# Kernel optimization log

Measured on AMD Instinct MI355X. Metric: run time of the kernel, lower is better.

## Reference

```python
import jax, jax.numpy as jnp
import numpy as np

B, H, W = 2, 256, 256


def _fwd_diff(x, ax):
    # forward difference with Neumann boundary (last entry = 0)
    pad = [(0, 0)] * x.ndim
    pad[ax] = (0, 1)
    return jnp.pad(jnp.diff(x, axis=ax), pad)


def _bwd_div(x, ax):
    # exact adjoint: <_fwd_diff(u), x> = -<u, _bwd_div(x)>
    sl = [slice(None)] * x.ndim
    sl[ax] = slice(0, -1)
    pad_end = [(0, 0)] * x.ndim
    pad_end[ax] = (0, 1)
    x0 = jnp.pad(x[tuple(sl)], pad_end)  # zero out last entry along ax
    pad_front = [(0, 0)] * x.ndim
    pad_front[ax] = (1, 0)
    shifted = jnp.pad(x0[tuple(sl)], pad_front)
    return x0 - shifted


def _grad(u):  # (B,H,W) -> (B,H,W,2)
    return jnp.stack([_fwd_diff(u, 1), _fwd_diff(u, 2)], axis=-1)


def _div(p):  # (B,H,W,2) -> (B,H,W)
    return _bwd_div(p[..., 0], 1) + _bwd_div(p[..., 1], 2)


def _sym_grad(v):  # (B,H,W,2) -> (B,H,W,3): (e11, e22, e12)
    v1, v2 = v[..., 0], v[..., 1]
    e11 = _fwd_diff(v1, 1)
    e22 = _fwd_diff(v2, 2)
    e12 = 0.5 * (_fwd_diff(v1, 2) + _fwd_diff(v2, 1))
    return jnp.stack([e11, e22, e12], axis=-1)


def _sym_div(q):  # adjoint of _sym_grad (with e12 counted twice)
    c1 = _bwd_div(q[..., 0], 1) + _bwd_div(q[..., 2], 2)
    c2 = _bwd_div(q[..., 2], 1) + _bwd_div(q[..., 1], 2)
    return jnp.stack([c1, c2], axis=-1)


def _proj_ball(p, alpha, weights):
    # pointwise projection onto {||p|| <= alpha} with weighted euclidean norm
    n = jnp.sqrt(jnp.sum(weights * p * p, axis=-1, keepdims=True))
    return p / jnp.maximum(1.0, n / alpha)


def _tgv_pdhg(u0, alpha0, alpha1, num_iters):
    # Chambolle-Pock PDHG for second-order TGV-regularized L2 denoising:
    #   min_u 0.5*||u - f||^2 + TGV_{alpha0,alpha1}(u)
    f = u0
    L = jnp.sqrt(12.0).astype(u0.dtype)  # ||K||^2 <= 12 for the TGV operator
    tau = 1.0 / L
    sigma = 1.0 / L
    v0 = jnp.zeros((*u0.shape, 2), u0.dtype)
    p0 = jnp.zeros((*u0.shape, 2), u0.dtype)  # matches p=zeros((*u.shape,2)) in the net
    q0 = jnp.zeros((*u0.shape, 3), u0.dtype)
    w1 = jnp.asarray([1.0, 1.0], u0.dtype)
    w2 = jnp.asarray([1.0, 1.0, 2.0], u0.dtype)  # off-diagonal counted twice

    @jax.checkpoint
    def step(carry, _):
        u, u_bar, v, v_bar, p, q = carry
        # dual ascent + projections
        p = _proj_ball(p + sigma * (_grad(u_bar) - v_bar), alpha1, w1)
        q = _proj_ball(q + sigma * _sym_grad(v_bar), alpha0, w2)
        # primal descent; prox of 0.5||u-f||^2
        u_new = (u + tau * _div(p) + tau * f) / (1.0 + tau)
        v_new = v + tau * (p + _sym_div(q))
        # over-relaxation (theta = 1)
        return (u_new, 2.0 * u_new - u, v_new, 2.0 * v_new - v, p, q), None

    carry0 = (u0, u0, v0, v0, p0, q0)
    (u_T, _, _, _, _, _), _ = jax.lax.scan(step, carry0, None, length=num_iters)
    return u_T


def setup_inputs() -> dict:
    key = jax.random.key(0)
    u = jax.random.normal(key, (B, H, W), dtype=jnp.float32)
    # the module hard-codes [0.1, 0.1] as the two regularisation parameters
    regularisation_params = jnp.array([0.1, 0.1], dtype=jnp.float32)
    return {"u": u, "regularisation_params": regularisation_params, "T": 128}


def reference(u, regularisation_params, T):
    alpha0 = regularisation_params[0]
    alpha1 = regularisation_params[1]
    return _tgv_pdhg(u, alpha0, alpha1, T)
```

## Files before the change

kernel.cpp:

```cpp
#include <hip/hip_runtime.h>
#include <math.h>


namespace {

typedef float v2f __attribute__((ext_vector_type(2)));

constexpr int kN = 2 * 256 * 256;
constexpr float kTau = 0.28867513459481287f;
constexpr float kSigma = kTau;
constexpr float kInv1pTau = 1.0f / (1.0f + kTau);

constexpr int RR = 32;
constexpr int RC = 48;
constexpr int A = RR * RC;
constexpr int PAD = 64;
constexpr int TILE_R = 16;
constexpr int TILE_C = 32;
constexpr int HALO = 8;
constexpr int NLAUNCH = 128 / HALO;
constexpr int NTHREADS = RR * (RC / 2);

__device__ __forceinline__ float4 ld4(const float* p) {
  return *reinterpret_cast<const float4*>(p);
}

template <bool M>
__device__ __forceinline__ void run8(
    float* ubS, float* vbS, float* p1S, float* p2S, float* q11S, float* q22S,
    float* q12S, const int rc, const int r, const float alpha0,
    const float alpha1, const float mD, const float mU, const v2f mR,
    const v2f mL, const v2f fI, v2f& u_, v2f& ub_, v2f& v1_, v2f& v2_,
    v2f& vb1_, v2f& vb2_, v2f& p1_, v2f& p2_, v2f& q11_, v2f& q22_,
    v2f& q12_) {
  for (int t = 0; t < HALO; ++t) {
    const bool pubD = (r >= t) && (r <= 31 - t);
    const bool actD = (r >= t) && (r <= 30 - t);
    const bool actP = (r >= t + 1) && (r <= 30 - t);

    if (pubD) {
      *reinterpret_cast<v2f*>(ubS + rc) = ub_;
      float4 vp;
      vp.x = vb1_.x; vp.y = vb2_.x; vp.z = vb1_.y; vp.w = vb2_.y;
      *reinterpret_cast<float4*>(vbS + 2 * rc) = vp;
    }
    __syncthreads();

    if (actD) {
      const float ubX = ubS[rc + 2];
      const v2f vbX = *reinterpret_cast<const v2f*>(vbS + 2 * (rc + 2));
      const v2f ubD = *reinterpret_cast<const v2f*>(ubS + rc + RC);
      const float4 vd = ld4(vbS + 2 * (rc + RC));
      v2f vb1D, vb2D;
      vb1D.x = vd.x; vb1D.y = vd.z;
      vb2D.x = vd.y; vb2D.y = vd.w;

      v2f ubr, vb1r, vb2r;
      ubr.x = ub_.y;   ubr.y = ubX;
      vb1r.x = vb1_.y; vb1r.y = vbX.x;
      vb2r.x = vb2_.y; vb2r.y = vbX.y;

      const v2f du1 = M ? mD * (ubD - ub_) : (ubD - ub_);
      const v2f du2 = M ? mR * (ubr - ub_) : (ubr - ub_);
      const v2f pn1 = p1_ + kSigma * (du1 - vb1_);
      const v2f pn2 = p2_ + kSigma * (du2 - vb2_);
      const v2f n2p = pn1 * pn1 + pn2 * pn2;
      v2f sp;
      sp.x = fminf(1.f, alpha1 * __builtin_amdgcn_rsqf(n2p.x));
      sp.y = fminf(1.f, alpha1 * __builtin_amdgcn_rsqf(n2p.y));
      p1_ = pn1 * sp;
      p2_ = pn2 * sp;

      const v2f e11 = M ? mD * (vb1D - vb1_) : (vb1D - vb1_);
      const v2f e22 = M ? mR * (vb2r - vb2_) : (vb2r - vb2_);
      const v2f e12 = M ? 0.5f * (mR * (vb1r - vb1_) + mD * (vb2D - vb2_))
                        : 0.5f * ((vb1r - vb1_) + (vb2D - vb2_));
      const v2f qn1 = q11_ + kSigma * e11;
      const v2f qn2 = q22_ + kSigma * e22;
      const v2f qn3 = q12_ + kSigma * e12;
      const v2f n2q = qn1 * qn1 + qn2 * qn2 + 2.f * (qn3 * qn3);
      v2f sq;
      sq.x = fminf(1.f, alpha0 * __builtin_amdgcn_rsqf(n2q.x));
      sq.y = fminf(1.f, alpha0 * __builtin_amdgcn_rsqf(n2q.y));
      q11_ = qn1 * sq;
      q22_ = qn2 * sq;
      q12_ = qn3 * sq;

      *reinterpret_cast<v2f*>(p1S + rc) = p1_;
      *reinterpret_cast<v2f*>(p2S + rc) = p2_;
      *reinterpret_cast<v2f*>(q11S + rc) = q11_;
      *reinterpret_cast<v2f*>(q22S + rc) = q22_;
      *reinterpret_cast<v2f*>(q12S + rc) = q12_;
    }
    __syncthreads();

    if (actP) {
      const v2f p1U = *reinterpret_cast<const v2f*>(p1S + rc - RC);
      const v2f q11U = *reinterpret_cast<const v2f*>(q11S + rc - RC);
      const v2f q12U = *reinterpret_cast<const v2f*>(q12S + rc - RC);
      const float p2Ls = p2S[rc - 1];
      const float q22Ls = q22S[rc - 1];
      const float q12Ls = q12S[rc - 1];

      v2f p2l, q22l, q12l;
      p2l.x = p2Ls;   p2l.y = p2_.x;
      q22l.x = q22Ls; q22l.y = q22_.x;
      q12l.x = q12Ls; q12l.y = q12_.x;

      const v2f divp = M ? (mD * p1_ + mR * p2_ - (mU * p1U + mL * p2l))
                         : (p1_ + p2_ - (p1U + p2l));
      const v2f un = (u_ + kTau * divp + fI) * kInv1pTau;
      ub_ = 2.f * un - u_;
      u_ = un;

      const v2f c1 = M ? (mD * q11_ + mR * q12_ - (mU * q11U + mL * q12l))
                       : (q11_ + q12_ - (q11U + q12l));
      const v2f c2 = M ? (mD * q12_ + mR * q22_ - (mU * q12U + mL * q22l))
                       : (q12_ + q22_ - (q12U + q22l));
      const v2f v1n = v1_ + kTau * (p1_ + c1);
      const v2f v2n = v2_ + kTau * (p2_ + c2);
      vb1_ = 2.f * v1n - v1_;
      v1_ = v1n;
      vb2_ = 2.f * v2n - v2_;
      v2_ = v2n;
    }
  }
}

__global__ __launch_bounds__(NTHREADS, 3) void tgv8_kernel(
    const float* __restrict__ f, const float* __restrict__ rp,
    float* __restrict__ ug, float* __restrict__ ws, int t0) {
  float* pr0 = ws + 0 * 2 * kN;
  float* pr1 = ws + 1 * 2 * kN;
  float* pr2 = ws + 2 * 2 * kN;
  float* pr3 = ws + 3 * 2 * kN;
  float* pr4 = ws + 4 * 2 * kN;

  __shared__ __align__(16) float smem[PAD + 8 * A + PAD];
  float* ubS = smem + PAD;
  float* vbS = ubS + A;
  float* p1S = vbS + 2 * A;
  float* p2S = p1S + A;
  float* q11S = p2S + A;
  float* q22S = q11S + A;
  float* q12S = q22S + A;

  const int lin = blockIdx.x + 8 * (blockIdx.y + 16 * blockIdx.z);
  const int j = ((lin & 7) << 5) | (lin >> 3);
  const int bz = j >> 7;
  const int by = (j >> 3) & 15;
  const int bx = j & 7;

  const int tid = threadIdx.x;
  const int r = tid / 24;
  const int c = (tid % 24) * 2;
  const int rc = r * RC + c;

  const int gi = by * TILE_R + r - HALO;
  const int gj = bx * TILE_C + c - HALO;
  const bool inImg = ((unsigned)gi < 256u) && ((unsigned)gj < 256u);
  const int base = bz * 65536 + gi * 256 + gj;

  const bool interior = (bx >= 1) && (bx <= 6) && (by >= 1) && (by <= 14);

  const float alpha0 = rp[0];
  const float alpha1 = rp[1];

  const float mD = (gi != 255) ? 1.f : 0.f;
  const float mU = (gi != 0) ? 1.f : 0.f;
  v2f mR, mL;
  mR.x = (gj + 0 != 255) ? 1.f : 0.f;
  mR.y = (gj + 1 != 255) ? 1.f : 0.f;
  mL.x = (gj != 0) ? 1.f : 0.f;
  mL.y = 1.f;

  v2f u_, ub_, v1_, v2_, vb1_, vb2_, p1_, p2_, q11_, q22_, q12_, f_;

#define LOADP(va, vb, src)                    \
  {                                           \
    const float4 t4 = ld4((src) + 2 * base);  \
    va.x = t4.x; vb.x = t4.y;                 \
    va.y = t4.z; vb.y = t4.w;                 \
  }
  if (inImg) {
    f_ = *reinterpret_cast<const v2f*>(f + base);
    if (t0 == 0) {
      u_ = f_; ub_ = f_;
      v1_ = 0.f; v2_ = 0.f; vb1_ = 0.f; vb2_ = 0.f;
      p1_ = 0.f; p2_ = 0.f; q11_ = 0.f; q22_ = 0.f; q12_ = 0.f;
    } else {
      LOADP(ub_, q12_, pr3)
      LOADP(vb1_, vb2_, pr0)
      LOADP(p1_, p2_, pr1)
      LOADP(q11_, q22_, pr2)
      u_ = *reinterpret_cast<const v2f*>(ug + base);
      LOADP(v1_, v2_, pr4)
    }
  } else {
    f_ = 0.f; u_ = 0.f; ub_ = 0.f;
    v1_ = 0.f; v2_ = 0.f; vb1_ = 0.f; vb2_ = 0.f;
    p1_ = 0.f; p2_ = 0.f; q11_ = 0.f; q22_ = 0.f; q12_ = 0.f;
  }
#undef LOADP

  const v2f fI = kTau * f_;

  if (interior) {
    run8<false>(ubS, vbS, p1S, p2S, q11S, q22S, q12S, rc, r, alpha0, alpha1,
                mD, mU, mR, mL, fI, u_, ub_, v1_, v2_, vb1_, vb2_, p1_, p2_,
                q11_, q22_, q12_);
  } else {
    run8<true>(ubS, vbS, p1S, p2S, q11S, q22S, q12S, rc, r, alpha0, alpha1,
               mD, mU, mR, mL, fI, u_, ub_, v1_, v2_, vb1_, vb2_, p1_, p2_,
               q11_, q22_, q12_);
  }

  if (r >= HALO && r < HALO + TILE_R && c >= HALO && c < HALO + TILE_C) {
#define STOREP(va, vb, dst)                              \
  {                                                      \
    float4 t4;                                           \
    t4.x = va.x; t4.y = vb.x; t4.z = va.y; t4.w = vb.y;  \
    *reinterpret_cast<float4*>((dst) + 2 * base) = t4;   \
  }
    *reinterpret_cast<v2f*>(ug + base) = u_;
    if (t0 != NLAUNCH - 1) {
      STOREP(vb1_, vb2_, pr0)
      STOREP(p1_, p2_, pr1)
      STOREP(q11_, q22_, pr2)
      STOREP(ub_, q12_, pr3)
      STOREP(v1_, v2_, pr4)
    }
#undef STOREP
  }
}

}

extern "C" void kernel_launch(void* const* d_in, const int* in_sizes, int n_in,
                              void* d_out, int out_size, void* d_ws,
                              size_t ws_size, hipStream_t stream) {
  const float* f = (const float*)d_in[0];
  const float* rp = (const float*)d_in[1];

  float* u = (float*)d_out;
  float* ws = (float*)d_ws;

  dim3 grid(256 / TILE_C, 256 / TILE_R, 2);
  for (int t = 0; t < NLAUNCH; ++t) {
    hipLaunchKernelGGL(tgv8_kernel, grid, dim3(NTHREADS), 0, stream, f, rp, u,
                       ws, t);
  }
}
```

Measured before the change: 199.3 us.

## Replace block barriers with neighbor-wave shared-memory flag synchronization

Replaces the two __syncthreads per time step with point-to-point flags in LDS: each wavefront publishes its step counter and spins only on the adjacent wavefront whose rows it reads. To map one row pair per wave, the block is widened to 32x32 threads with 8 idle lanes per row and launch bounds lowered to 1 block per CU. This removes full-block barrier stalls but wastes a quarter of the lanes, lowers occupancy, and relies on volatile spin-waits and waitcnt ordering being correct.

```diff
diff --git a/kernel.cpp b/kernel.cpp
--- a/kernel.cpp
+++ b/kernel.cpp
@@ -19,7 +19,7 @@
 constexpr int TILE_C = 32;
 constexpr int HALO = 8;
 constexpr int NLAUNCH = 128 / HALO;
-constexpr int NTHREADS = RR * (RC / 2);
+constexpr int NTHREADS = 32 * 32;
 
 __device__ __forceinline__ float4 ld4(const float* p) {
   return *reinterpret_cast<const float4*>(p);
@@ -28,15 +28,16 @@
 template <bool M>
 __device__ __forceinline__ void run8(
     float* ubS, float* vbS, float* p1S, float* p2S, float* q11S, float* q22S,
-    float* q12S, const int rc, const int r, const float alpha0,
-    const float alpha1, const float mD, const float mU, const v2f mR,
-    const v2f mL, const v2f fI, v2f& u_, v2f& ub_, v2f& v1_, v2f& v2_,
-    v2f& vb1_, v2f& vb2_, v2f& p1_, v2f& p2_, v2f& q11_, v2f& q22_,
+    float* q12S, volatile int* vA, volatile int* vB, const int w,
+    const int lane, const bool active, const int rc, const int r,
+    const float alpha0, const float alpha1, const float mD, const float mU,
+    const v2f mR, const v2f mL, const v2f fI, v2f& u_, v2f& ub_, v2f& v1_,
+    v2f& v2_, v2f& vb1_, v2f& vb2_, v2f& p1_, v2f& p2_, v2f& q11_, v2f& q22_,
     v2f& q12_) {
   for (int t = 0; t < HALO; ++t) {
-    const bool pubD = (r >= t) && (r <= 31 - t);
-    const bool actD = (r >= t) && (r <= 30 - t);
-    const bool actP = (r >= t + 1) && (r <= 30 - t);
+    const bool pubD = active && (r >= t) && (r <= 31 - t);
+    const bool actD = active && (r >= t) && (r <= 30 - t);
+    const bool actP = active && (r >= t + 1) && (r <= 30 - t);
 
     if (pubD) {
       *reinterpret_cast<v2f*>(ubS + rc) = ub_;
@@ -44,7 +45,13 @@
       vp.x = vb1_.x; vp.y = vb2_.x; vp.z = vb1_.y; vp.w = vb2_.y;
       *reinterpret_cast<float4*>(vbS + 2 * rc) = vp;
     }
-    __syncthreads();
+    asm volatile("s_waitcnt lgkmcnt(0)" ::: "memory");
+    if (lane == 0) vA[w] = t;
+    if (w < 15) {
+      while (vA[w + 1] < t) {
+      }
+    }
+    __builtin_amdgcn_sched_barrier(0);
 
     if (actD) {
       const float ubX = ubS[rc + 2];
@@ -92,7 +99,13 @@
       *reinterpret_cast<v2f*>(q22S + rc) = q22_;
       *reinterpret_cast<v2f*>(q12S + rc) = q12_;
     }
-    __syncthreads();
+    asm volatile("s_waitcnt lgkmcnt(0)" ::: "memory");
+    if (lane == 0) vB[w] = t;
+    if (w > 0) {
+      while (vB[w - 1] < t) {
+      }
+    }
+    __builtin_amdgcn_sched_barrier(0);
 
     if (actP) {
       const v2f p1U = *reinterpret_cast<const v2f*>(p1S + rc - RC);
@@ -127,7 +140,7 @@
   }
 }
 
-__global__ __launch_bounds__(NTHREADS, 3) void tgv8_kernel(
+__global__ __launch_bounds__(NTHREADS, 1) void tgv8_kernel(
     const float* __restrict__ f, const float* __restrict__ rp,
     float* __restrict__ ug, float* __restrict__ ws, int t0) {
   float* pr0 = ws + 0 * 2 * kN;
@@ -137,6 +150,8 @@
   float* pr4 = ws + 4 * 2 * kN;
 
   __shared__ __align__(16) float smem[PAD + 8 * A + PAD];
+  __shared__ int flagA[16];
+  __shared__ int flagB[16];
   float* ubS = smem + PAD;
   float* vbS = ubS + A;
   float* p1S = vbS + 2 * A;
@@ -152,13 +167,23 @@
   const int bx = j & 7;
 
   const int tid = threadIdx.x;
-  const int r = tid / 24;
-  const int c = (tid % 24) * 2;
+  const int r = tid >> 5;
+  const int s = tid & 31;
+  const bool active = (s < 24);
+  const int c = s * 2;
   const int rc = r * RC + c;
+  const int w = tid >> 6;
+  const int lane = tid & 63;
+
+  if (tid < 16) {
+    flagA[tid] = -1;
+    flagB[tid] = -1;
+  }
+  __syncthreads();
 
   const int gi = by * TILE_R + r - HALO;
   const int gj = bx * TILE_C + c - HALO;
-  const bool inImg = ((unsigned)gi < 256u) && ((unsigned)gj < 256u);
+  const bool inImg = active && ((unsigned)gi < 256u) && ((unsigned)gj < 256u);
   const int base = bz * 65536 + gi * 256 + gj;
 
   const bool interior = (bx >= 1) && (bx <= 6) && (by >= 1) && (by <= 14);
@@ -206,13 +231,13 @@
   const v2f fI = kTau * f_;
 
   if (interior) {
-    run8<false>(ubS, vbS, p1S, p2S, q11S, q22S, q12S, rc, r, alpha0, alpha1,
-                mD, mU, mR, mL, fI, u_, ub_, v1_, v2_, vb1_, vb2_, p1_, p2_,
-                q11_, q22_, q12_);
+    run8<false>(ubS, vbS, p1S, p2S, q11S, q22S, q12S, flagA, flagB, w, lane,
+                active, rc, r, alpha0, alpha1, mD, mU, mR, mL, fI, u_, ub_,
+                v1_, v2_, vb1_, vb2_, p1_, p2_, q11_, q22_, q12_);
   } else {
-    run8<true>(ubS, vbS, p1S, p2S, q11S, q22S, q12S, rc, r, alpha0, alpha1,
-               mD, mU, mR, mL, fI, u_, ub_, v1_, v2_, vb1_, vb2_, p1_, p2_,
-               q11_, q22_, q12_);
+    run8<true>(ubS, vbS, p1S, p2S, q11S, q22S, q12S, flagA, flagB, w, lane,
+               active, rc, r, alpha0, alpha1, mD, mU, mR, mL, fI, u_, ub_,
+               v1_, v2_, vb1_, vb2_, p1_, p2_, q11_, q22_, q12_);
   }
 
   if (r >= HALO && r < HALO + TILE_R && c >= HALO && c < HALO + TILE_C) {
```

New measurement: 235.0 us. 1.18x slower.
